# Performance work log

Measured on AMD Instinct MI355X. Metric: run time of the kernel, lower is better.

## Reference

```python
import jax, jax.numpy as jnp
import numpy as np
import math

BLOCK_SIZE = 128  # config.block_size


def setup_inputs() -> dict:
    key = jax.random.key(0)
    k1, k2, k3 = jax.random.split(key, 3)
    B, H, S, D = 2, 12, 4096, 64
    return {
        "query_layer": jax.random.normal(k1, (B, H, S, D), dtype=jnp.float32),
        "key_layer": jax.random.normal(k2, (B, H, S, D), dtype=jnp.float32),
        "value_layer": jax.random.normal(k3, (B, H, S, D), dtype=jnp.float32),
        "attention_mask": jnp.zeros((B, 1, 1, S), dtype=jnp.float32),
    }


def reference(query_layer, key_layer, value_layer, attention_mask):
    d = query_layer.shape[-1]
    # [B,H,S,S] attention scores
    scores = jnp.einsum("bhqd,bhkd->bhqk", query_layer, key_layer) / math.sqrt(d)
    scores = scores + attention_mask
    # Faithful to source: the bottom-right block is OVERWRITTEN with
    # tril(ones, -1).T * finfo.min  (0 on/below diag, min strictly above)
    bs = BLOCK_SIZE
    causal_mask = jnp.tril(jnp.ones((bs, bs), dtype=scores.dtype), k=-1).T
    causal_mask = causal_mask * jnp.finfo(scores.dtype).min
    scores = scores.at[..., -bs:, -bs:].set(causal_mask)
    probs = jax.nn.softmax(scores, axis=-1)
    # dropout is identity in eval mode
    return jnp.einsum("bhqk,bhkd->bhqd", probs, value_layer)
```

## Files before the change

### kernel.cpp

```cpp
#include <hip/hip_runtime.h>

#define S_LEN 4096
#define DH    64
#define BQ    128
#define BK    64
#define NTILE (S_LEN / BK)
#define QBLKS (S_LEN / BQ)
#define NBH   24
#define NHEADS 12

typedef __attribute__((ext_vector_type(8))) short short8;
typedef __attribute__((ext_vector_type(4))) short short4v;
typedef __attribute__((ext_vector_type(4))) float f32x4;
typedef __attribute__((ext_vector_type(4))) unsigned uint4v;

#define KSTR 72
#define VSTR 72
#define LOG2E 1.44269504088896f
#define MCONST (-12.99718425f)

#define NKCH (NBH * S_LEN * DH / 8)

__device__ __forceinline__ short f2bf(float x) {
    unsigned u = __builtin_bit_cast(unsigned, x);
    return (short)((u + 0x8000u) >> 16);
}

typedef __attribute__((address_space(1))) const unsigned int guint;
typedef __attribute__((address_space(3))) unsigned int luint;
__device__ __forceinline__ void g2l16(const short* g, short* l) {
    __builtin_amdgcn_global_load_lds((guint*)g, (luint*)l, 16, 0, 0);
}

__device__ __forceinline__ void swap32(unsigned &a, unsigned &b) {
    asm("v_permlane32_swap_b32 %0, %1" : "+v"(a), "+v"(b));
}
__device__ __forceinline__ void swap16(unsigned &a, unsigned &b) {
    asm("v_permlane16_swap_b32 %0, %1" : "+v"(a), "+v"(b));
}

__global__ __launch_bounds__(256)
void prepass(const float* __restrict__ K, const float* __restrict__ V,
             const float* __restrict__ M, short* __restrict__ Kf,
             short* __restrict__ Vtf, float* __restrict__ Mf)
{
    __shared__ __align__(16) short K_lds[BK * KSTR];
    __shared__ __align__(16) short Vt_lds[DH * VSTR];

    const int tid = threadIdx.x;
    const int bh  = blockIdx.x >> 6;
    const int t   = blockIdx.x & 63;
    const size_t base = ((size_t)bh * S_LEN + (size_t)t * BK) * DH;

    #pragma unroll
    for (int it = 0; it < 4; ++it) {
        int idx = tid + 256 * it;
        int row = idx >> 4, c4 = idx & 15;
        float4 v = *(const float4*)(K + base + (size_t)row * DH + 4 * c4);
        short4v b4 = { f2bf(v.x), f2bf(v.y), f2bf(v.z), f2bf(v.w) };
        *(short4v*)&K_lds[row * KSTR + 4 * c4] = b4;
    }
    {
        int kb = tid >> 4, db = tid & 15;
        const float* vp = V + base + (size_t)(4 * kb) * DH + 4 * db;
        float4 r0 = *(const float4*)(vp);
        float4 r1 = *(const float4*)(vp + DH);
        float4 r2 = *(const float4*)(vp + 2 * DH);
        float4 r3 = *(const float4*)(vp + 3 * DH);
        short4v c0 = { f2bf(r0.x), f2bf(r1.x), f2bf(r2.x), f2bf(r3.x) };
        short4v c1 = { f2bf(r0.y), f2bf(r1.y), f2bf(r2.y), f2bf(r3.y) };
        short4v c2 = { f2bf(r0.z), f2bf(r1.z), f2bf(r2.z), f2bf(r3.z) };
        short4v c3 = { f2bf(r0.w), f2bf(r1.w), f2bf(r2.w), f2bf(r3.w) };
        *(short4v*)&Vt_lds[(4 * db + 0) * VSTR + 4 * kb] = c0;
        *(short4v*)&Vt_lds[(4 * db + 1) * VSTR + 4 * kb] = c1;
        *(short4v*)&Vt_lds[(4 * db + 2) * VSTR + 4 * kb] = c2;
        *(short4v*)&Vt_lds[(4 * db + 3) * VSTR + 4 * kb] = c3;
    }
    __syncthreads();

    const size_t obase = (size_t)(bh * NTILE + t) * 4096;
    #pragma unroll
    for (int e = 0; e < 2; ++e) {
        int ci = tid + 256 * e;
        int lane = ci & 63, n = lane & 15, q = lane >> 4;
        {
            int kt = (ci >> 6) & 1, mt = ci >> 7;
            short8 f = *(const short8*)&K_lds[(16 * mt + n) * KSTR + 32 * kt + 8 * q];
            *(short8*)&Kf[obase + (size_t)ci * 8] = f;
        }
        {
            int d = (ci >> 6) & 3, kt2 = (ci >> 8) & 1;
            short8 g2 = *(const short8*)&Vt_lds[(16 * d + n) * VSTR + 32 * kt2 + 8 * q];
            *(short8*)&Vtf[obase + (size_t)ci * 8] = g2;
        }
    }
    if ((bh % NHEADS) == 0 && tid < 16) {
        int b_idx = bh / NHEADS;
        float4 mv = *(const float4*)(M + (size_t)b_idx * S_LEN + t * BK + 4 * tid);
        mv.x = mv.x * LOG2E + MCONST;
        mv.y = mv.y * LOG2E + MCONST;
        mv.z = mv.z * LOG2E + MCONST;
        mv.w = mv.w * LOG2E + MCONST;
        *(float4*)&Mf[(size_t)b_idx * S_LEN + t * BK + 4 * tid] = mv;
    }
}

__global__ __launch_bounds__(256, 3)
void fa10(const float* __restrict__ Q, const short* __restrict__ Kf,
          const short* __restrict__ Vtf, const float* __restrict__ Mf,
          float* __restrict__ O)
{
    __shared__ __align__(16) short Ks[2][4096];
    __shared__ __align__(16) short Vs[2][4096];

    const int tid  = threadIdx.x;
    const int w    = tid >> 6;
    const int lane = tid & 63;
    const int n    = lane & 15;
    const int quad = lane >> 4;

    const int bid  = blockIdx.x;
    const int x    = bid & 7;
    const int g    = bid >> 3;
    const int bh   = x + 8 * (g >> 5);
    const int qblk = g & 31;
    const bool special = (qblk == QBLKS - 1);

    const size_t base  = (size_t)bh * S_LEN * DH;
    const int    b_idx = bh / NHEADS;

    const float QSCALE = 0.125f * LOG2E;
    const int q0 = qblk * BQ + w * 32;
    short8 qf[2][2];
    #pragma unroll
    for (int s = 0; s < 2; ++s) {
        const float* qp = Q + base + (size_t)(q0 + 16 * s + n) * DH;
        #pragma unroll
        for (int kt = 0; kt < 2; ++kt) {
            const float* p = qp + 32 * kt + 8 * quad;
            float4 a = *(const float4*)p;
            float4 b = *(const float4*)(p + 4);
            short8 f;
            f[0] = f2bf(a.x * QSCALE); f[1] = f2bf(a.y * QSCALE);
            f[2] = f2bf(a.z * QSCALE); f[3] = f2bf(a.w * QSCALE);
            f[4] = f2bf(b.x * QSCALE); f[5] = f2bf(b.y * QSCALE);
            f[6] = f2bf(b.z * QSCALE); f[7] = f2bf(b.w * QSCALE);
            qf[s][kt] = f;
        }
    }

    f32x4 o[4][2];
    #pragma unroll
    for (int d = 0; d < 4; ++d)
        #pragma unroll
        for (int s = 0; s < 2; ++s) o[d][s] = (f32x4){0.f, 0.f, 0.f, 0.f};
    f32x4 lsum[2] = { (f32x4){0.f,0.f,0.f,0.f}, (f32x4){0.f,0.f,0.f,0.f} };

    const short8 ONES = { 0x3F80, 0x3F80, 0x3F80, 0x3F80,
                          0x3F80, 0x3F80, 0x3F80, 0x3F80 };
    const float* mrow = Mf + (size_t)b_idx * S_LEN;
    const short* Kg = Kf  + (size_t)(bh * NTILE) * 4096;
    const short* Vg = Vtf + (size_t)(bh * NTILE) * 4096;

    #pragma unroll
    for (int i = 0; i < 2; ++i) {
        int c = 2 * w + i;
        g2l16(Kg + c * 512 + lane * 8, &Ks[0][c * 512]);
        g2l16(Vg + c * 512 + lane * 8, &Vs[0][c * 512]);
    }
    __syncthreads();

    for (int t = 0; t < NTILE; ++t) {
        const bool sp = special && t >= NTILE - 2;
        const int  cur = t & 1, nxt = cur ^ 1;

        if (t + 1 < NTILE) {
            const short* kg = Kg + (size_t)(t + 1) * 4096;
            const short* vg = Vg + (size_t)(t + 1) * 4096;
            #pragma unroll
            for (int i = 0; i < 2; ++i) {
                int c = 2 * w + i;
                g2l16(kg + c * 512 + lane * 8, &Ks[nxt][c * 512]);
                g2l16(vg + c * 512 + lane * 8, &Vs[nxt][c * 512]);
            }
        }

        #pragma unroll
        for (int h = 0; h < 2; ++h) {
            short8 pf[2];
            if (!sp) {
                unsigned u[2][2][2];
                #pragma unroll
                for (int mm = 0; mm < 2; ++mm) {
                    const int mt = 2 * h + mm;
                    short8 k0 = *(const short8*)&Ks[cur][(2 * mt    ) * 512 + lane * 8];
                    short8 k1 = *(const short8*)&Ks[cur][(2 * mt + 1) * 512 + lane * 8];
                    f32x4 mk = *(const f32x4*)(mrow + t * BK + 16 * mt + 4 * quad);
                    #pragma unroll
                    for (int s = 0; s < 2; ++s) {
                        f32x4 c = mk;
                        c = __builtin_amdgcn_mfma_f32_16x16x32_bf16(k0, qf[s][0], c, 0, 0, 0);
                        c = __builtin_amdgcn_mfma_f32_16x16x32_bf16(k1, qf[s][1], c, 0, 0, 0);
                        float p0 = __builtin_amdgcn_exp2f(c[0]);
                        float p1 = __builtin_amdgcn_exp2f(c[1]);
                        float p2 = __builtin_amdgcn_exp2f(c[2]);
                        float p3 = __builtin_amdgcn_exp2f(c[3]);
                        unsigned d0 = __builtin_amdgcn_perm(
                            __builtin_bit_cast(unsigned, p1),
                            __builtin_bit_cast(unsigned, p0), 0x07060302u);
                        unsigned d1 = __builtin_amdgcn_perm(
                            __builtin_bit_cast(unsigned, p3),
                            __builtin_bit_cast(unsigned, p2), 0x07060302u);
                        u[mm][s][0] = d0;
                        u[mm][s][1] = d1;
                    }
                }
                #pragma unroll
                for (int s = 0; s < 2; ++s) {
                    unsigned X0 = u[0][s][0], Y0 = u[1][s][0];
                    unsigned X1 = u[0][s][1], Y1 = u[1][s][1];
                    swap32(X0, Y0); swap16(X0, Y0);
                    swap32(X1, Y1); swap16(X1, Y1);
                    uint4v pc = (uint4v){X0, X1, Y0, Y1};
                    pf[s] = __builtin_bit_cast(short8, pc);
                }
            } else {
                #pragma unroll
                for (int s = 0; s < 2; ++s) {
                    const int qs = q0 + 16 * s + n;
                    const int kb = BK * t + 32 * h + 8 * quad;
                    unsigned c0 = (kb     <= qs ? 0x3900u : 0u) | (kb + 1 <= qs ? 0x39000000u : 0u);
                    unsigned c1 = (kb + 2 <= qs ? 0x3900u : 0u) | (kb + 3 <= qs ? 0x39000000u : 0u);
                    unsigned c2 = (kb + 4 <= qs ? 0x3900u : 0u) | (kb + 5 <= qs ? 0x39000000u : 0u);
                    unsigned c3 = (kb + 6 <= qs ? 0x3900u : 0u) | (kb + 7 <= qs ? 0x39000000u : 0u);
                    uint4v pc = (uint4v){c0, c1, c2, c3};
                    pf[s] = __builtin_bit_cast(short8, pc);
                }
            }

            lsum[0] = __builtin_amdgcn_mfma_f32_16x16x32_bf16(ONES, pf[0], lsum[0], 0, 0, 0);
            lsum[1] = __builtin_amdgcn_mfma_f32_16x16x32_bf16(ONES, pf[1], lsum[1], 0, 0, 0);

            #pragma unroll
            for (int d = 0; d < 4; ++d) {
                short8 vf = *(const short8*)&Vs[cur][(h * 4 + d) * 512 + lane * 8];
                o[d][0] = __builtin_amdgcn_mfma_f32_16x16x32_bf16(vf, pf[0], o[d][0], 0, 0, 0);
                o[d][1] = __builtin_amdgcn_mfma_f32_16x16x32_bf16(vf, pf[1], o[d][1], 0, 0, 0);
            }
        }

        __syncthreads();
    }

    #pragma unroll
    for (int s = 0; s < 2; ++s) {
        float inv = 1.0f / lsum[s][0];
        int qg = q0 + 16 * s + n;
        float* op = O + base + (size_t)qg * DH;
        #pragma unroll
        for (int d = 0; d < 4; ++d) {
            f32x4 r = o[d][s] * inv;
            *(f32x4*)(op + 16 * d + 4 * quad) = r;
        }
    }
}

extern "C" void kernel_launch(void* const* d_in, const int* in_sizes, int n_in,
                              void* d_out, int out_size, void* d_ws, size_t ws_size,
                              hipStream_t stream) {
    const float* Q = (const float*)d_in[0];
    const float* K = (const float*)d_in[1];
    const float* V = (const float*)d_in[2];
    const float* M = (const float*)d_in[3];
    float* O = (float*)d_out;

    short* Kf  = (short*)d_ws;
    short* Vtf = Kf + (size_t)NKCH * 8;
    float* Mf  = (float*)(Vtf + (size_t)NKCH * 8);

    prepass<<<dim3(NBH * NTILE), dim3(256), 0, stream>>>(K, V, M, Kf, Vtf, Mf);
    fa10<<<dim3(NBH * QBLKS), dim3(256), 0, stream>>>(Q, Kf, Vtf, Mf, O);
}
```

Before: 230.0 us.

## Split query block across eight waves with 16 rows each instead of four

```diff
diff --git a/kernel.cpp b/kernel.cpp
--- a/kernel.cpp
+++ b/kernel.cpp
@@ -105,8 +105,8 @@
     }
 }
 
-__global__ __launch_bounds__(256, 3)
-void fa10(const float* __restrict__ Q, const short* __restrict__ Kf,
+__global__ __launch_bounds__(512, 3)
+void fa11(const float* __restrict__ Q, const short* __restrict__ Kf,
           const short* __restrict__ Vtf, const float* __restrict__ Mf,
           float* __restrict__ O)
 {
@@ -130,11 +130,10 @@
     const int    b_idx = bh / NHEADS;
 
     const float QSCALE = 0.125f * LOG2E;
-    const int q0 = qblk * BQ + w * 32;
-    short8 qf[2][2];
-    #pragma unroll
-    for (int s = 0; s < 2; ++s) {
-        const float* qp = Q + base + (size_t)(q0 + 16 * s + n) * DH;
+    const int qbase = qblk * BQ + w * 16;
+    short8 qf[2];
+    {
+        const float* qp = Q + base + (size_t)(qbase + n) * DH;
         #pragma unroll
         for (int kt = 0; kt < 2; ++kt) {
             const float* p = qp + 32 * kt + 8 * quad;
@@ -145,16 +144,14 @@
             f[2] = f2bf(a.z * QSCALE); f[3] = f2bf(a.w * QSCALE);
             f[4] = f2bf(b.x * QSCALE); f[5] = f2bf(b.y * QSCALE);
             f[6] = f2bf(b.z * QSCALE); f[7] = f2bf(b.w * QSCALE);
-            qf[s][kt] = f;
-        }
-    }
-
-    f32x4 o[4][2];
+            qf[kt] = f;
+        }
+    }
+
+    f32x4 o[4];
     #pragma unroll
-    for (int d = 0; d < 4; ++d)
-        #pragma unroll
-        for (int s = 0; s < 2; ++s) o[d][s] = (f32x4){0.f, 0.f, 0.f, 0.f};
-    f32x4 lsum[2] = { (f32x4){0.f,0.f,0.f,0.f}, (f32x4){0.f,0.f,0.f,0.f} };
+    for (int d = 0; d < 4; ++d) o[d] = (f32x4){0.f, 0.f, 0.f, 0.f};
+    f32x4 lsum = (f32x4){0.f, 0.f, 0.f, 0.f};
 
     const short8 ONES = { 0x3F80, 0x3F80, 0x3F80, 0x3F80,
                           0x3F80, 0x3F80, 0x3F80, 0x3F80 };
@@ -162,12 +159,8 @@
     const short* Kg = Kf  + (size_t)(bh * NTILE) * 4096;
     const short* Vg = Vtf + (size_t)(bh * NTILE) * 4096;
 
-    #pragma unroll
-    for (int i = 0; i < 2; ++i) {
-        int c = 2 * w + i;
-        g2l16(Kg + c * 512 + lane * 8, &Ks[0][c * 512]);
-        g2l16(Vg + c * 512 + lane * 8, &Vs[0][c * 512]);
-    }
+    g2l16(Kg + w * 512 + lane * 8, &Ks[0][w * 512]);
+    g2l16(Vg + w * 512 + lane * 8, &Vs[0][w * 512]);
     __syncthreads();
 
     for (int t = 0; t < NTILE; ++t) {
@@ -175,91 +168,69 @@
         const int  cur = t & 1, nxt = cur ^ 1;
 
         if (t + 1 < NTILE) {
-            const short* kg = Kg + (size_t)(t + 1) * 4096;
-            const short* vg = Vg + (size_t)(t + 1) * 4096;
-            #pragma unroll
-            for (int i = 0; i < 2; ++i) {
-                int c = 2 * w + i;
-                g2l16(kg + c * 512 + lane * 8, &Ks[nxt][c * 512]);
-                g2l16(vg + c * 512 + lane * 8, &Vs[nxt][c * 512]);
-            }
+            g2l16(Kg + (size_t)(t + 1) * 4096 + w * 512 + lane * 8, &Ks[nxt][w * 512]);
+            g2l16(Vg + (size_t)(t + 1) * 4096 + w * 512 + lane * 8, &Vs[nxt][w * 512]);
         }
 
         #pragma unroll
         for (int h = 0; h < 2; ++h) {
-            short8 pf[2];
+            short8 pf;
             if (!sp) {
-                unsigned u[2][2][2];
+                unsigned u[2][2];
                 #pragma unroll
                 for (int mm = 0; mm < 2; ++mm) {
                     const int mt = 2 * h + mm;
                     short8 k0 = *(const short8*)&Ks[cur][(2 * mt    ) * 512 + lane * 8];
                     short8 k1 = *(const short8*)&Ks[cur][(2 * mt + 1) * 512 + lane * 8];
-                    f32x4 mk = *(const f32x4*)(mrow + t * BK + 16 * mt + 4 * quad);
-                    #pragma unroll
-                    for (int s = 0; s < 2; ++s) {
-                        f32x4 c = mk;
-                        c = __builtin_amdgcn_mfma_f32_16x16x32_bf16(k0, qf[s][0], c, 0, 0, 0);
-                        c = __builtin_amdgcn_mfma_f32_16x16x32_bf16(k1, qf[s][1], c, 0, 0, 0);
-                        float p0 = __builtin_amdgcn_exp2f(c[0]);
-                        float p1 = __builtin_amdgcn_exp2f(c[1]);
-                        float p2 = __builtin_amdgcn_exp2f(c[2]);
-                        float p3 = __builtin_amdgcn_exp2f(c[3]);
-                        unsigned d0 = __builtin_amdgcn_perm(
-                            __builtin_bit_cast(unsigned, p1),
-                            __builtin_bit_cast(unsigned, p0), 0x07060302u);
-                        unsigned d1 = __builtin_amdgcn_perm(
-                            __builtin_bit_cast(unsigned, p3),
-                            __builtin_bit_cast(unsigned, p2), 0x07060302u);
-                        u[mm][s][0] = d0;
-                        u[mm][s][1] = d1;
-                    }
+                    f32x4 c = *(const f32x4*)(mrow + t * BK + 16 * mt + 4 * quad);
+                    c = __builtin_amdgcn_mfma_f32_16x16x32_bf16(k0, qf[0], c, 0, 0, 0);
+                    c = __builtin_amdgcn_mfma_f32_16x16x32_bf16(k1, qf[1], c, 0, 0, 0);
+                    float p0 = __builtin_amdgcn_exp2f(c[0]);
+                    float p1 = __builtin_amdgcn_exp2f(c[1]);
+                    float p2 = __builtin_amdgcn_exp2f(c[2]);
+                    float p3 = __builtin_amdgcn_exp2f(c[3]);
+                    u[mm][0] = __builtin_amdgcn_perm(
+                        __builtin_bit_cast(unsigned, p1),
+                        __builtin_bit_cast(unsigned, p0), 0x07060302u);
+                    u[mm][1] = __builtin_amdgcn_perm(
+                        __builtin_bit_cast(unsigned, p3),
+                        __builtin_bit_cast(unsigned, p2), 0x07060302u);
                 }
-                #pragma unroll
-                for (int s = 0; s < 2; ++s) {
-                    unsigned X0 = u[0][s][0], Y0 = u[1][s][0];
-                    unsigned X1 = u[0][s][1], Y1 = u[1][s][1];
-                    swap32(X0, Y0); swap16(X0, Y0);
-                    swap32(X1, Y1); swap16(X1, Y1);
-                    uint4v pc = (uint4v){X0, X1, Y0, Y1};
-                    pf[s] = __builtin_bit_cast(short8, pc);
-                }
+                unsigned X0 = u[0][0], Y0 = u[1][0];
+                unsigned X1 = u[0][1], Y1 = u[1][1];
+                swap32(X0, Y0); swap16(X0, Y0);
+                swap32(X1, Y1); swap16(X1, Y1);
+                uint4v pc = (uint4v){X0, X1, Y0, Y1};
+                pf = __builtin_bit_cast(short8, pc);
             } else {
-                #pragma unroll
-                for (int s = 0; s < 2; ++s) {
-                    const int qs = q0 + 16 * s + n;
-                    const int kb = BK * t + 32 * h + 8 * quad;
-                    unsigned c0 = (kb     <= qs ? 0x3900u : 0u) | (kb + 1 <= qs ? 0x39000000u : 0u);
-                    unsigned c1 = (kb + 2 <= qs ? 0x3900u : 0u) | (kb + 3 <= qs ? 0x39000000u : 0u);
-                    unsigned c2 = (kb + 4 <= qs ? 0x3900u : 0u) | (kb + 5 <= qs ? 0x39000000u : 0u);
-                    unsigned c3 = (kb + 6 <= qs ? 0x3900u : 0u) | (kb + 7 <= qs ? 0x39000000u : 0u);
-                    uint4v pc = (uint4v){c0, c1, c2, c3};
-                    pf[s] = __builtin_bit_cast(short8, pc);
-                }
+                const int qs = qbase + n;
+                const int kb = BK * t + 32 * h + 8 * quad;
+                unsigned c0 = (kb     <= qs ? 0x3900u : 0u) | (kb + 1 <= qs ? 0x39000000u : 0u);
+                unsigned c1 = (kb + 2 <= qs ? 0x3900u : 0u) | (kb + 3 <= qs ? 0x39000000u : 0u);
+                unsigned c2 = (kb + 4 <= qs ? 0x3900u : 0u) | (kb + 5 <= qs ? 0x39000000u : 0u);
+                unsigned c3 = (kb + 6 <= qs ? 0x3900u : 0u) | (kb + 7 <= qs ? 0x39000000u : 0u);
+                uint4v pc = (uint4v){c0, c1, c2, c3};
+                pf = __builtin_bit_cast(short8, pc);
             }
 
-            lsum[0] = __builtin_amdgcn_mfma_f32_16x16x32_bf16(ONES, pf[0], lsum[0], 0, 0, 0);
-            lsum[1] = __builtin_amdgcn_mfma_f32_16x16x32_bf16(ONES, pf[1], lsum[1], 0, 0, 0);
+            lsum = __builtin_amdgcn_mfma_f32_16x16x32_bf16(ONES, pf, lsum, 0, 0, 0);
 
             #pragma unroll
             for (int d = 0; d < 4; ++d) {
                 short8 vf = *(const short8*)&Vs[cur][(h * 4 + d) * 512 + lane * 8];
-                o[d][0] = __builtin_amdgcn_mfma_f32_16x16x32_bf16(vf, pf[0], o[d][0], 0, 0, 0);
-                o[d][1] = __builtin_amdgcn_mfma_f32_16x16x32_bf16(vf, pf[1], o[d][1], 0, 0, 0);
+                o[d] = __builtin_amdgcn_mfma_f32_16x16x32_bf16(vf, pf, o[d], 0, 0, 0);
             }
         }
 
         __syncthreads();
     }
 
-    #pragma unroll
-    for (int s = 0; s < 2; ++s) {
-        float inv = 1.0f / lsum[s][0];
-        int qg = q0 + 16 * s + n;
-        float* op = O + base + (size_t)qg * DH;
+    {
+        float inv = 1.0f / lsum[0];
+        float* op = O + base + (size_t)(qbase + n) * DH;
         #pragma unroll
         for (int d = 0; d < 4; ++d) {
-            f32x4 r = o[d][s] * inv;
+            f32x4 r = o[d] * inv;
             *(f32x4*)(op + 16 * d + 4 * quad) = r;
         }
     }
@@ -279,5 +250,5 @@
     float* Mf  = (float*)(Vtf + (size_t)NKCH * 8);
 
     prepass<<<dim3(NBH * NTILE), dim3(256), 0, stream>>>(K, V, M, Kf, Vtf, Mf);
-    fa10<<<dim3(NBH * QBLKS), dim3(256), 0, stream>>>(Q, Kf, Vtf, Mf, O);
-}
+    fa11<<<dim3(NBH * QBLKS), dim3(512), 0, stream>>>(Q, Kf, Vtf, Mf, O);
+}
```

After: 233.5 us. About the same (+1.5%).

## Load K tiles directly from global into registers, double-buffered across unrolled iterations

Applied to the files above, without the earlier changes.

```diff
diff --git a/kernel.cpp b/kernel.cpp
--- a/kernel.cpp
+++ b/kernel.cpp
@@ -106,11 +106,10 @@
 }
 
 __global__ __launch_bounds__(256, 3)
-void fa10(const float* __restrict__ Q, const short* __restrict__ Kf,
+void fa14(const float* __restrict__ Q, const short* __restrict__ Kf,
           const short* __restrict__ Vtf, const float* __restrict__ Mf,
           float* __restrict__ O)
 {
-    __shared__ __align__(16) short Ks[2][4096];
     __shared__ __align__(16) short Vs[2][4096];
 
     const int tid  = threadIdx.x;
@@ -162,95 +161,108 @@
     const short* Kg = Kf  + (size_t)(bh * NTILE) * 4096;
     const short* Vg = Vtf + (size_t)(bh * NTILE) * 4096;
 
+    short8 ka[8], kb[8];
     #pragma unroll
     for (int i = 0; i < 2; ++i) {
         int c = 2 * w + i;
-        g2l16(Kg + c * 512 + lane * 8, &Ks[0][c * 512]);
         g2l16(Vg + c * 512 + lane * 8, &Vs[0][c * 512]);
     }
+    #pragma unroll
+    for (int c = 0; c < 8; ++c)
+        ka[c] = *(const short8*)(Kg + c * 512 + lane * 8);
     __syncthreads();
 
-    for (int t = 0; t < NTILE; ++t) {
-        const bool sp = special && t >= NTILE - 2;
-        const int  cur = t & 1, nxt = cur ^ 1;
-
-        if (t + 1 < NTILE) {
-            const short* kg = Kg + (size_t)(t + 1) * 4096;
-            const short* vg = Vg + (size_t)(t + 1) * 4096;
-            #pragma unroll
-            for (int i = 0; i < 2; ++i) {
-                int c = 2 * w + i;
-                g2l16(kg + c * 512 + lane * 8, &Ks[nxt][c * 512]);
-                g2l16(vg + c * 512 + lane * 8, &Vs[nxt][c * 512]);
-            }
-        }
-
-        #pragma unroll
-        for (int h = 0; h < 2; ++h) {
-            short8 pf[2];
-            if (!sp) {
-                unsigned u[2][2][2];
-                #pragma unroll
-                for (int mm = 0; mm < 2; ++mm) {
-                    const int mt = 2 * h + mm;
-                    short8 k0 = *(const short8*)&Ks[cur][(2 * mt    ) * 512 + lane * 8];
-                    short8 k1 = *(const short8*)&Ks[cur][(2 * mt + 1) * 512 + lane * 8];
-                    f32x4 mk = *(const f32x4*)(mrow + t * BK + 16 * mt + 4 * quad);
-                    #pragma unroll
-                    for (int s = 0; s < 2; ++s) {
-                        f32x4 c = mk;
-                        c = __builtin_amdgcn_mfma_f32_16x16x32_bf16(k0, qf[s][0], c, 0, 0, 0);
-                        c = __builtin_amdgcn_mfma_f32_16x16x32_bf16(k1, qf[s][1], c, 0, 0, 0);
-                        float p0 = __builtin_amdgcn_exp2f(c[0]);
-                        float p1 = __builtin_amdgcn_exp2f(c[1]);
-                        float p2 = __builtin_amdgcn_exp2f(c[2]);
-                        float p3 = __builtin_amdgcn_exp2f(c[3]);
-                        unsigned d0 = __builtin_amdgcn_perm(
-                            __builtin_bit_cast(unsigned, p1),
-                            __builtin_bit_cast(unsigned, p0), 0x07060302u);
-                        unsigned d1 = __builtin_amdgcn_perm(
-                            __builtin_bit_cast(unsigned, p3),
-                            __builtin_bit_cast(unsigned, p2), 0x07060302u);
-                        u[mm][s][0] = d0;
-                        u[mm][s][1] = d1;
-                    }
-                }
-                #pragma unroll
-                for (int s = 0; s < 2; ++s) {
-                    unsigned X0 = u[0][s][0], Y0 = u[1][s][0];
-                    unsigned X1 = u[0][s][1], Y1 = u[1][s][1];
-                    swap32(X0, Y0); swap16(X0, Y0);
-                    swap32(X1, Y1); swap16(X1, Y1);
-                    uint4v pc = (uint4v){X0, X1, Y0, Y1};
-                    pf[s] = __builtin_bit_cast(short8, pc);
-                }
-            } else {
-                #pragma unroll
-                for (int s = 0; s < 2; ++s) {
-                    const int qs = q0 + 16 * s + n;
-                    const int kb = BK * t + 32 * h + 8 * quad;
-                    unsigned c0 = (kb     <= qs ? 0x3900u : 0u) | (kb + 1 <= qs ? 0x39000000u : 0u);
-                    unsigned c1 = (kb + 2 <= qs ? 0x3900u : 0u) | (kb + 3 <= qs ? 0x39000000u : 0u);
-                    unsigned c2 = (kb + 4 <= qs ? 0x3900u : 0u) | (kb + 5 <= qs ? 0x39000000u : 0u);
-                    unsigned c3 = (kb + 6 <= qs ? 0x3900u : 0u) | (kb + 7 <= qs ? 0x39000000u : 0u);
-                    uint4v pc = (uint4v){c0, c1, c2, c3};
-                    pf[s] = __builtin_bit_cast(short8, pc);
-                }
-            }
-
-            lsum[0] = __builtin_amdgcn_mfma_f32_16x16x32_bf16(ONES, pf[0], lsum[0], 0, 0, 0);
-            lsum[1] = __builtin_amdgcn_mfma_f32_16x16x32_bf16(ONES, pf[1], lsum[1], 0, 0, 0);
-
-            #pragma unroll
-            for (int d = 0; d < 4; ++d) {
-                short8 vf = *(const short8*)&Vs[cur][(h * 4 + d) * 512 + lane * 8];
-                o[d][0] = __builtin_amdgcn_mfma_f32_16x16x32_bf16(vf, pf[0], o[d][0], 0, 0, 0);
-                o[d][1] = __builtin_amdgcn_mfma_f32_16x16x32_bf16(vf, pf[1], o[d][1], 0, 0, 0);
-            }
-        }
-
-        __syncthreads();
-    }
+#define FA14_TILE(T, KC, KN)                                                   \
+    {                                                                          \
+        const int t   = (T);                                                   \
+        const bool sp = special && t >= NTILE - 2;                             \
+        const int cur = t & 1, nxt = cur ^ 1;                                  \
+        const int tn  = (t + 1 < NTILE) ? t + 1 : t;                           \
+            \
+        {                                                                      \
+            const short* vg = Vg + (size_t)tn * 4096;                          \
+            _Pragma("unroll")                                                  \
+            for (int i = 0; i < 2; ++i) {                                      \
+                int c = 2 * w + i;                                             \
+                g2l16(vg + c * 512 + lane * 8, &Vs[nxt][c * 512]);             \
+            }                                                                  \
+            const short* kg = Kg + (size_t)tn * 4096;                          \
+            _Pragma("unroll")                                                  \
+            for (int c = 0; c < 8; ++c)                                        \
+                KN[c] = *(const short8*)(kg + c * 512 + lane * 8);             \
+        }                                                                      \
+          \
+        _Pragma("unroll")                                                      \
+        for (int h = 0; h < 2; ++h) {                                          \
+            short8 pf[2];                                                      \
+            if (!sp) {                                                         \
+                unsigned u[2][2][2];                                           \
+                _Pragma("unroll")                                              \
+                for (int mm = 0; mm < 2; ++mm) {                               \
+                    const int mt = 2 * h + mm;                                 \
+                    short8 k0 = KC[2 * mt];                                    \
+                    short8 k1 = KC[2 * mt + 1];                                \
+                    f32x4 mk = *(const f32x4*)(mrow + t * BK + 16 * mt + 4 * quad); \
+                    _Pragma("unroll")                                          \
+                    for (int s = 0; s < 2; ++s) {                              \
+                        f32x4 c = mk;                                          \
+                        c = __builtin_amdgcn_mfma_f32_16x16x32_bf16(k0, qf[s][0], c, 0, 0, 0); \
+                        c = __builtin_amdgcn_mfma_f32_16x16x32_bf16(k1, qf[s][1], c, 0, 0, 0); \
+                        float p0 = __builtin_amdgcn_exp2f(c[0]);               \
+                        float p1 = __builtin_amdgcn_exp2f(c[1]);               \
+                        float p2 = __builtin_amdgcn_exp2f(c[2]);               \
+                        float p3 = __builtin_amdgcn_exp2f(c[3]);               \
+                        unsigned d0 = __builtin_amdgcn_perm(                   \
+                            __builtin_bit_cast(unsigned, p1),                  \
+                            __builtin_bit_cast(unsigned, p0), 0x07060302u);    \
+                        unsigned d1 = __builtin_amdgcn_perm(                   \
+                            __builtin_bit_cast(unsigned, p3),                  \
+                            __builtin_bit_cast(unsigned, p2), 0x07060302u);    \
+                        u[mm][s][0] = d0;                                      \
+                        u[mm][s][1] = d1;                                      \
+                    }                                                          \
+                }                                                              \
+                _Pragma("unroll")                                              \
+                for (int s = 0; s < 2; ++s) {                                  \
+                    unsigned X0 = u[0][s][0], Y0 = u[1][s][0];                 \
+                    unsigned X1 = u[0][s][1], Y1 = u[1][s][1];                 \
+                    swap32(X0, Y0); swap16(X0, Y0);                            \
+                    swap32(X1, Y1); swap16(X1, Y1);                            \
+                    uint4v pc = (uint4v){X0, X1, Y0, Y1};                      \
+                    pf[s] = __builtin_bit_cast(short8, pc);                    \
+                }                                                              \
+            } else {                                                           \
+                _Pragma("unroll")                                              \
+                for (int s = 0; s < 2; ++s) {                                  \
+                    const int qs = q0 + 16 * s + n;                            \
+                    const int kbk = BK * t + 32 * h + 8 * quad;                \
+                    unsigned c0 = (kbk     <= qs ? 0x3900u : 0u) | (kbk + 1 <= qs ? 0x39000000u : 0u); \
+                    unsigned c1 = (kbk + 2 <= qs ? 0x3900u : 0u) | (kbk + 3 <= qs ? 0x39000000u : 0u); \
+                    unsigned c2 = (kbk + 4 <= qs ? 0x3900u : 0u) | (kbk + 5 <= qs ? 0x39000000u : 0u); \
+                    unsigned c3 = (kbk + 6 <= qs ? 0x3900u : 0u) | (kbk + 7 <= qs ? 0x39000000u : 0u); \
+                    uint4v pc = (uint4v){c0, c1, c2, c3};                      \
+                    pf[s] = __builtin_bit_cast(short8, pc);                    \
+                }                                                              \
+            }                                                                  \
+            lsum[0] = __builtin_amdgcn_mfma_f32_16x16x32_bf16(ONES, pf[0], lsum[0], 0, 0, 0); \
+            lsum[1] = __builtin_amdgcn_mfma_f32_16x16x32_bf16(ONES, pf[1], lsum[1], 0, 0, 0); \
+            _Pragma("unroll")                                                  \
+            for (int d = 0; d < 4; ++d) {                                      \
+                short8 vf = *(const short8*)&Vs[cur][(h * 4 + d) * 512 + lane * 8]; \
+                o[d][0] = __builtin_amdgcn_mfma_f32_16x16x32_bf16(vf, pf[0], o[d][0], 0, 0, 0); \
+                o[d][1] = __builtin_amdgcn_mfma_f32_16x16x32_bf16(vf, pf[1], o[d][1], 0, 0, 0); \
+            }                                                                  \
+        }                                                                      \
+           \
+        __syncthreads();                                                       \
+    }
+
+    #pragma unroll 1
+    for (int uu = 0; uu < NTILE / 2; ++uu) {
+        FA14_TILE(2 * uu,     ka, kb)
+        FA14_TILE(2 * uu + 1, kb, ka)
+    }
+#undef FA14_TILE
 
     #pragma unroll
     for (int s = 0; s < 2; ++s) {
@@ -279,5 +291,5 @@
     float* Mf  = (float*)(Vtf + (size_t)NKCH * 8);
 
     prepass<<<dim3(NBH * NTILE), dim3(256), 0, stream>>>(K, V, M, Kf, Vtf, Mf);
-    fa10<<<dim3(NBH * QBLKS), dim3(256), 0, stream>>>(Q, Kf, Vtf, Mf, O);
-}
+    fa14<<<dim3(NBH * QBLKS), dim3(256), 0, stream>>>(Q, Kf, Vtf, Mf, O);
+}
```

Result: no change. 232.7 us (+1.2%).
